# Kernel tuning notes

Hardware: AMD Instinct MI355X
Metric: run time of the kernel (lower is better)

## Reference

```python
import jax, jax.numpy as jnp
import numpy as np

DIM = 1024
LN_EPS = 1e-5

def _layernorm(x, w, b):
    m = jnp.mean(x, axis=-1, keepdims=True)
    v = jnp.mean((x - m) ** 2, axis=-1, keepdims=True)
    return (x - m) * jax.lax.rsqrt(v + LN_EPS) * w + b

def _linear(x, w, b):
    # torch Linear: w is (out, in)
    return jnp.einsum('bsd,od->bso', x, w) + b

def setup_inputs() -> dict:
    key = jax.random.key(0)
    ks = jax.random.split(key, 8)
    d = DIM
    s = 0.02
    return {
        'x': jax.random.normal(ks[0], (4, 4096, d), dtype=jnp.float32),
        'ln1_w': jnp.ones((d,), jnp.float32), 'ln1_b': jnp.zeros((d,), jnp.float32),
        'ln2_w': jnp.ones((d,), jnp.float32), 'ln2_b': jnp.zeros((d,), jnp.float32),
        'gate_w': jax.random.normal(ks[1], (d, d), jnp.float32) * s,
        'gate_b': jnp.zeros((d,), jnp.float32),
        'val_w': jax.random.normal(ks[2], (d, d), jnp.float32) * s,
        'val_b': jnp.zeros((d,), jnp.float32),
        'ffn1_w': jax.random.normal(ks[3], (4 * d, d), jnp.float32) * s,
        'ffn1_b': jnp.zeros((4 * d,), jnp.float32),
        'ffn2_w': jax.random.normal(ks[4], (d, 4 * d), jnp.float32) * s,
        'ffn2_b': jnp.zeros((d,), jnp.float32),
    }

def reference(x, ln1_w, ln1_b, ln2_w, ln2_b, gate_w, gate_b, val_w, val_b, ffn1_w, ffn1_b, ffn2_w, ffn2_b):
    batch, seq_len, dim = x.shape
    h = _layernorm(x, ln1_w, ln1_b)
    g = jax.nn.sigmoid(_linear(h, gate_w, gate_b))
    v = _linear(h, val_w, val_b)
    cumsum_v = jnp.cumsum(g * v, axis=1)
    cumsum_g = jnp.cumsum(g, axis=1) + 1e-6
    position = jnp.arange(1, seq_len + 1, dtype=x.dtype)[None, :, None]  # [1,S,1]
    mem = cumsum_v / (jnp.sqrt(cumsum_g) * jnp.sqrt(position / seq_len + 0.1))
    x = x + mem
    h2 = _layernorm(x, ln2_w, ln2_b)
    ff = _linear(jax.nn.gelu(_linear(h2, ffn1_w, ffn1_b), approximate=False), ffn2_w, ffn2_b)
    return x + ff
```

## Files before the change

kernel.cpp:

```cpp
#include <hip/hip_runtime.h>
#include <cstdint>
#include <cstddef>

#define DIMD 1024
#define SEQ  4096
#define BATCH 4
#define MTOT (BATCH*SEQ)
#define NCHUNK 64
#define CLEN   64

typedef __attribute__((ext_vector_type(8))) short short8;
typedef __attribute__((ext_vector_type(4))) float floatx4;

__device__ __forceinline__ unsigned short f2bf(float f){
  unsigned u = __float_as_uint(f);
  u += 0x7fffu + ((u >> 16) & 1u);
  return (unsigned short)(u >> 16);
}
__device__ __forceinline__ float bf2f(unsigned short u){
  return __uint_as_float((unsigned)u << 16);
}

__device__ __forceinline__ void async16(const void* g, void* l){
  __builtin_amdgcn_global_load_lds(
      (const __attribute__((address_space(1))) void*)g,
      (__attribute__((address_space(3))) void*)l, 16, 0, 0);
}

__global__ void f32_to_bf16_kernel(const float* __restrict__ in,
                                   unsigned short* __restrict__ out, int n){
  int i = (blockIdx.x * 256 + threadIdx.x) * 4;
  if (i < n){
    float4 v = *(const float4*)(in + i);
    uint2 o;
    o.x = (unsigned)f2bf(v.x) | ((unsigned)f2bf(v.y) << 16);
    o.y = (unsigned)f2bf(v.z) | ((unsigned)f2bf(v.w) << 16);
    *(uint2*)(out + i) = o;
  }
}

__global__ __launch_bounds__(256)
void ln_kernel(const float* __restrict__ X, const float* __restrict__ w,
               const float* __restrict__ b, unsigned short* __restrict__ H){
  const int row = blockIdx.x;
  const int tid = threadIdx.x;
  const float4 xv = ((const float4*)(X + (size_t)row * DIMD))[tid];
  float s  = xv.x + xv.y + xv.z + xv.w;
  float ss = xv.x*xv.x + xv.y*xv.y + xv.z*xv.z + xv.w*xv.w;
  #pragma unroll
  for (int o = 32; o; o >>= 1){
    s  += __shfl_down(s, o);
    ss += __shfl_down(ss, o);
  }
  __shared__ float ps[4], pss[4], mv[2];
  const int wid = tid >> 6, lane = tid & 63;
  if (lane == 0){ ps[wid] = s; pss[wid] = ss; }
  __syncthreads();
  if (tid == 0){
    float S1 = ps[0]+ps[1]+ps[2]+ps[3];
    float S2 = pss[0]+pss[1]+pss[2]+pss[3];
    float m = S1 * (1.0f / DIMD);
    float var = S2 * (1.0f / DIMD) - m*m;
    mv[0] = m; mv[1] = rsqrtf(var + 1e-5f);
  }
  __syncthreads();
  const float m = mv[0], rs = mv[1];
  const float4 wv = ((const float4*)w)[tid];
  const float4 bv = ((const float4*)b)[tid];
  float o0 = (xv.x - m) * rs * wv.x + bv.x;
  float o1 = (xv.y - m) * rs * wv.y + bv.y;
  float o2 = (xv.z - m) * rs * wv.z + bv.z;
  float o3 = (xv.w - m) * rs * wv.w + bv.w;
  uint2 o;
  o.x = (unsigned)f2bf(o0) | ((unsigned)f2bf(o1) << 16);
  o.y = (unsigned)f2bf(o2) | ((unsigned)f2bf(o3) << 16);
  ((uint2*)(H + (size_t)row * DIMD))[tid] = o;
}

template<int EPI>
__global__ __launch_bounds__(256, 4)
void gemm_bf16(const unsigned short* __restrict__ A, int lda,
               const unsigned short* __restrict__ Bw, int ldb,
               const float* __restrict__ bias, const float* __restrict__ bias2,
               void* __restrict__ OutP, void* __restrict__ Out2P,
               int ldc, int grid_n, int K)
{
  __shared__ unsigned short Alds[2][128*32];
  __shared__ unsigned short Blds[2][128*32];
  const int tid = threadIdx.x;
  const int bid = ((int)blockIdx.x & 7) * ((int)gridDim.x >> 3) + ((int)blockIdx.x >> 3);
  const int bm = bid / grid_n, bn = bid % grid_n;
  const int row0 = bm * 128, col0 = bn * 128;
  const int wid = tid >> 6, lane = tid & 63;
  const int wr = wid >> 1, wc = wid & 1;
  const int l15 = lane & 15, kh = (lane >> 4) * 8, rq = lane >> 4;

  const int idx0 = tid * 8;
  const int idx1 = 2048 + tid * 8;
  const int ar0 = idx0 >> 5, ac0 = idx0 & 31;
  const int ar1 = idx1 >> 5, ac1 = idx1 & 31;

  floatx4 acc[4][4];
  #pragma unroll
  for (int m = 0; m < 4; ++m)
    #pragma unroll
    for (int n = 0; n < 4; ++n)
      acc[m][n] = (floatx4){0.f, 0.f, 0.f, 0.f};

  auto stage = [&](int b, int k0){
    async16(A  + (size_t)(row0 + ar0) * lda + k0 + ac0, (char*)(&Alds[b][0]) + idx0*2);
    async16(A  + (size_t)(row0 + ar1) * lda + k0 + ac1, (char*)(&Alds[b][0]) + idx1*2);
    async16(Bw + (size_t)(col0 + ar0) * ldb + k0 + ac0, (char*)(&Blds[b][0]) + idx0*2);
    async16(Bw + (size_t)(col0 + ar1) * ldb + k0 + ac1, (char*)(&Blds[b][0]) + idx1*2);
  };
  auto compute = [&](int b){
    short8 af[4], bfr[4];
    #pragma unroll
    for (int m = 0; m < 4; ++m)
      af[m] = *(const short8*)(&Alds[b][(wr*64 + m*16 + l15)*32 + kh]);
    #pragma unroll
    for (int n = 0; n < 4; ++n)
      bfr[n] = *(const short8*)(&Blds[b][(wc*64 + n*16 + l15)*32 + kh]);
    #pragma unroll
    for (int m = 0; m < 4; ++m)
      #pragma unroll
      for (int n = 0; n < 4; ++n)
        acc[m][n] = __builtin_amdgcn_mfma_f32_16x16x32_bf16(af[m], bfr[n], acc[m][n], 0, 0, 0);
  };

  const int nt = K >> 5;
  stage(0, 0);
  __syncthreads();
  int cur = 0;
  for (int t = 0; t < nt - 1; ++t){
    stage(cur ^ 1, (t + 1) << 5);
    compute(cur);
    __syncthreads();
    cur ^= 1;
  }
  compute(cur);

  #pragma unroll
  for (int n = 0; n < 4; ++n){
    const int col = col0 + wc*64 + n*16 + l15;
    float bs;
    if constexpr (EPI == 4)      bs = 0.f;
    else if constexpr (EPI == 5) bs = (col < 1024) ? bias[col] : bias2[col - 1024];
    else                         bs = bias[col];
    #pragma unroll
    for (int m = 0; m < 4; ++m){
      const int rowb = row0 + wr*64 + m*16 + rq*4;
      #pragma unroll
      for (int j = 0; j < 4; ++j){
        const size_t o = (size_t)(rowb + j) * ldc + col;
        float val = acc[m][n][j] + bs;
        if constexpr (EPI == 2){
          ((unsigned short*)OutP)[o] = f2bf(0.5f * val * (1.f + erff(val * 0.70710678118f)));
        } else if constexpr (EPI == 3){
          float* O = (float*)OutP;
          O[o] = val + O[o];
        } else if constexpr (EPI == 4){
          float* O = (float*)OutP;
          O[o] = val + O[o];
        } else {
          if (col < 1024){
            ((unsigned short*)OutP)[(size_t)(rowb + j) * 1024 + col] =
                f2bf(1.f / (1.f + expf(-val)));
          } else {
            ((unsigned short*)Out2P)[(size_t)(rowb + j) * 1024 + (col - 1024)] =
                f2bf(val);
          }
        }
      }
    }
  }
}

__global__ __launch_bounds__(256)
void scan_sums(const unsigned short* __restrict__ G, const unsigned short* __restrict__ V,
               float* __restrict__ SG, float* __restrict__ SGV){
  const int bc = blockIdx.x;
  const int d  = blockIdx.y * 256 + threadIdx.x;
  const int b = bc >> 6, c = bc & 63;
  size_t base = ((size_t)b * SEQ + (size_t)c * CLEN) * DIMD + d;
  float sg = 0.f, sgv = 0.f;
  for (int i = 0; i < CLEN; ++i){
    float g = bf2f(G[base + (size_t)i * DIMD]);
    float v = bf2f(V[base + (size_t)i * DIMD]);
    sg += g; sgv += g * v;
  }
  SG[(size_t)bc * DIMD + d] = sg;
  SGV[(size_t)bc * DIMD + d] = sgv;
}

__global__ __launch_bounds__(256)
void scan_prefix(float* __restrict__ SG, float* __restrict__ SGV){
  const int b = blockIdx.x;
  const int d = blockIdx.y * 256 + threadIdx.x;
  float rg = 0.f, rgv = 0.f;
  for (int c = 0; c < NCHUNK; ++c){
    size_t i = ((size_t)(b * NCHUNK + c)) * DIMD + d;
    float tg = SG[i], tv = SGV[i];
    SG[i] = rg; SGV[i] = rgv;
    rg += tg; rgv += tv;
  }
}

__global__ __launch_bounds__(256)
void scan_final(const unsigned short* __restrict__ G, const unsigned short* __restrict__ V,
                const float* __restrict__ SG, const float* __restrict__ SGV,
                const float* __restrict__ X, float* __restrict__ X2){
  const int bc = blockIdx.x;
  const int d  = blockIdx.y * 256 + threadIdx.x;
  const int b = bc >> 6, c = bc & 63;
  size_t base = ((size_t)b * SEQ + (size_t)c * CLEN) * DIMD + d;
  float rg  = SG[(size_t)bc * DIMD + d];
  float rgv = SGV[(size_t)bc * DIMD + d];
  for (int i = 0; i < CLEN; ++i){
    size_t idx = base + (size_t)i * DIMD;
    float g = bf2f(G[idx]), v = bf2f(V[idx]);
    rg += g; rgv += g * v;
    int s = c * CLEN + i;
    float pf = (float)(s + 1) * (1.0f / SEQ) + 0.1f;
    float mem = rgv * rsqrtf((rg + 1e-6f) * pf);
    X2[idx] = X[idx] + mem;
  }
}

extern "C" void kernel_launch(void* const* d_in, const int* in_sizes, int n_in,
                              void* d_out, int out_size, void* d_ws, size_t ws_size,
                              hipStream_t stream)
{
  const float* x     = (const float*)d_in[0];
  const float* ln1w  = (const float*)d_in[1];
  const float* ln1b  = (const float*)d_in[2];
  const float* ln2w  = (const float*)d_in[3];
  const float* ln2b  = (const float*)d_in[4];
  const float* gatew = (const float*)d_in[5];
  const float* gateb = (const float*)d_in[6];
  const float* valw  = (const float*)d_in[7];
  const float* valb  = (const float*)d_in[8];
  const float* f1w   = (const float*)d_in[9];
  const float* f1b   = (const float*)d_in[10];
  const float* f2w   = (const float*)d_in[11];
  const float* f2b   = (const float*)d_in[12];
  float* out = (float*)d_out;

  const size_t MB = 1024u * 1024u;
  const size_t baseNeed = (size_t)(32+32+32+2+2+8+8)*MB + 2u*BATCH*NCHUNK*DIMD*4 + 4096;
  const bool bigT = (baseNeed + 64u*MB) <= ws_size;

  char* ws = (char*)d_ws;
  size_t off = 0;
  auto alloc = [&](size_t bytes) -> char* {
    char* p = ws + off; off += (bytes + 255) & ~(size_t)255; return p;
  };
  unsigned short* H  = (unsigned short*)alloc((size_t)MTOT * DIMD * 2);
  unsigned short* G  = (unsigned short*)alloc((size_t)MTOT * DIMD * 2);
  unsigned short* V  = (unsigned short*)alloc((size_t)MTOT * DIMD * 2);
  if (bigT) alloc(64u * MB);
  unsigned short* T  = G;
  unsigned short* WGV= (unsigned short*)alloc((size_t)2 * DIMD * DIMD * 2);
  unsigned short* W1 = (unsigned short*)alloc((size_t)4 * DIMD * DIMD * 2);
  unsigned short* W2 = (unsigned short*)alloc((size_t)4 * DIMD * DIMD * 2);
  float* SG  = (float*)alloc((size_t)BATCH * NCHUNK * DIMD * 4);
  float* SGV = (float*)alloc((size_t)BATCH * NCHUNK * DIMD * 4);

  if (off > ws_size) return;

  f32_to_bf16_kernel<<<DIMD*DIMD/1024, 256, 0, stream>>>(gatew, WGV, DIMD*DIMD);
  f32_to_bf16_kernel<<<DIMD*DIMD/1024, 256, 0, stream>>>(valw,  WGV + (size_t)DIMD*DIMD, DIMD*DIMD);
  f32_to_bf16_kernel<<<4*DIMD*DIMD/1024, 256, 0, stream>>>(f1w, W1, 4*DIMD*DIMD);
  f32_to_bf16_kernel<<<4*DIMD*DIMD/1024, 256, 0, stream>>>(f2w, W2, 4*DIMD*DIMD);

  ln_kernel<<<MTOT, 256, 0, stream>>>(x, ln1w, ln1b, H);

  gemm_bf16<5><<<(MTOT/128)*(2048/128), 256, 0, stream>>>(
      H, DIMD, WGV, DIMD, gateb, valb, G, V, 2048, 2048/128, DIMD);

  scan_sums  <<<dim3(BATCH*NCHUNK, DIMD/256), 256, 0, stream>>>(G, V, SG, SGV);
  scan_prefix<<<dim3(BATCH, DIMD/256),        256, 0, stream>>>(SG, SGV);
  scan_final <<<dim3(BATCH*NCHUNK, DIMD/256), 256, 0, stream>>>(G, V, SG, SGV, x, out);

  ln_kernel<<<MTOT, 256, 0, stream>>>(out, ln2w, ln2b, H);

  if (bigT){
    for (int c = 0; c < 2; ++c)
      gemm_bf16<2><<<(MTOT/128)*(2048/128), 256, 0, stream>>>(
          H, DIMD, W1 + (size_t)c*2048*DIMD, DIMD, f1b + c*2048, nullptr,
          T + (size_t)c*2048, nullptr, 4*DIMD, 2048/128, DIMD);
    gemm_bf16<3><<<(MTOT/128)*(DIMD/128), 256, 0, stream>>>(
        T, 4*DIMD, W2, 4*DIMD, f2b, nullptr, out, nullptr, DIMD, DIMD/128, 4*DIMD);
  } else {
    for (int c = 0; c < 2; ++c){
      const unsigned short* W1c = W1 + (size_t)c * 2048 * DIMD;
      const unsigned short* W2c = W2 + (size_t)c * 2048;
      gemm_bf16<2><<<(MTOT/128)*(2048/128), 256, 0, stream>>>(
          H, DIMD, W1c, DIMD, f1b + c*2048, nullptr, T, nullptr, 2048, 2048/128, DIMD);
      if (c == 0)
        gemm_bf16<3><<<(MTOT/128)*(DIMD/128), 256, 0, stream>>>(
            T, 2048, W2c, 4*DIMD, f2b, nullptr, out, nullptr, DIMD, DIMD/128, 2048);
      else
        gemm_bf16<4><<<(MTOT/128)*(DIMD/128), 256, 0, stream>>>(
            T, 2048, W2c, 4*DIMD, nullptr, nullptr, out, nullptr, DIMD, DIMD/128, 2048);
    }
  }
}
```

Baseline: 585.6 us.

## Replace 128x128 GEMM with 256x256 tile, 8-wave kernel using swizzled LDS

The bf16 MFMA GEMM moves from 128x128x32 tiles with 4 waves to 256x256x64 tiles with 8 waves. LDS loads now use an XOR swizzle to avoid bank conflicts, and the next K-tile is staged during the first quarter of compute, with s_setprio raised around the MFMA bursts. Larger tiles cut global and LDS traffic per FLOP. In exchange each wave holds 32 accumulators, which raises register pressure and lowers occupancy, and the grid has fewer blocks. With bigT, the FFN1 GEMM also runs as one launch instead of two.

```diff
diff --git a/kernel.cpp b/kernel.cpp
--- a/kernel.cpp
+++ b/kernel.cpp
@@ -78,78 +78,102 @@
 }
 
 template<int EPI>
-__global__ __launch_bounds__(256, 4)
-void gemm_bf16(const unsigned short* __restrict__ A, int lda,
-               const unsigned short* __restrict__ Bw, int ldb,
-               const float* __restrict__ bias, const float* __restrict__ bias2,
-               void* __restrict__ OutP, void* __restrict__ Out2P,
-               int ldc, int grid_n, int K)
+__global__ __launch_bounds__(512, 2)
+void gemm256(const unsigned short* __restrict__ A, int lda,
+             const unsigned short* __restrict__ Bw, int ldb,
+             const float* __restrict__ bias, const float* __restrict__ bias2,
+             void* __restrict__ OutP, void* __restrict__ Out2P,
+             int ldc, int grid_n, int K)
 {
-  __shared__ unsigned short Alds[2][128*32];
-  __shared__ unsigned short Blds[2][128*32];
+  __shared__ char lds[2][2][32*1024];
   const int tid = threadIdx.x;
   const int bid = ((int)blockIdx.x & 7) * ((int)gridDim.x >> 3) + ((int)blockIdx.x >> 3);
   const int bm = bid / grid_n, bn = bid % grid_n;
-  const int row0 = bm * 128, col0 = bn * 128;
+  const int row0 = bm * 256, col0 = bn * 256;
   const int wid = tid >> 6, lane = tid & 63;
-  const int wr = wid >> 1, wc = wid & 1;
-  const int l15 = lane & 15, kh = (lane >> 4) * 8, rq = lane >> 4;
-
-  const int idx0 = tid * 8;
-  const int idx1 = 2048 + tid * 8;
-  const int ar0 = idx0 >> 5, ac0 = idx0 & 31;
-  const int ar1 = idx1 >> 5, ac1 = idx1 & 31;
-
-  floatx4 acc[4][4];
+  const int wr = wid >> 2, wc = wid & 3;
+  const int l15 = lane & 15, rq = lane >> 4, l7 = lane & 7;
+
+  const int sbase = ((rq ^ (l7 & 3)) << 4) | (((l7 >> 2) & 1) << 6);
+
+  const int st_r  = tid >> 3;
+  const int st_sl = (tid & 7) ^ (st_r & 7);
+  const int st_ldsoff = tid * 16;
+
+  const unsigned short* Asrc = A  + (size_t)(row0 + st_r) * lda + st_sl * 8;
+  const unsigned short* Bsrc = Bw + (size_t)(col0 + st_r) * ldb + st_sl * 8;
+
+  floatx4 acc[8][4];
   #pragma unroll
-  for (int m = 0; m < 4; ++m)
+  for (int m = 0; m < 8; ++m)
     #pragma unroll
     for (int n = 0; n < 4; ++n)
       acc[m][n] = (floatx4){0.f, 0.f, 0.f, 0.f};
 
-  auto stage = [&](int b, int k0){
-    async16(A  + (size_t)(row0 + ar0) * lda + k0 + ac0, (char*)(&Alds[b][0]) + idx0*2);
-    async16(A  + (size_t)(row0 + ar1) * lda + k0 + ac1, (char*)(&Alds[b][0]) + idx1*2);
-    async16(Bw + (size_t)(col0 + ar0) * ldb + k0 + ac0, (char*)(&Blds[b][0]) + idx0*2);
-    async16(Bw + (size_t)(col0 + ar1) * ldb + k0 + ac1, (char*)(&Blds[b][0]) + idx1*2);
+  auto stage = [&](int buf, int k0){
+    #pragma unroll
+    for (int i = 0; i < 4; ++i)
+      async16(Asrc + (size_t)(i * 64) * lda + k0, &lds[buf][0][i * 8192 + st_ldsoff]);
+    #pragma unroll
+    for (int i = 0; i < 4; ++i)
+      async16(Bsrc + (size_t)(i * 64) * ldb + k0, &lds[buf][1][i * 8192 + st_ldsoff]);
   };
-  auto compute = [&](int b){
-    short8 af[4], bfr[4];
-    #pragma unroll
-    for (int m = 0; m < 4; ++m)
-      af[m] = *(const short8*)(&Alds[b][(wr*64 + m*16 + l15)*32 + kh]);
-    #pragma unroll
-    for (int n = 0; n < 4; ++n)
-      bfr[n] = *(const short8*)(&Blds[b][(wc*64 + n*16 + l15)*32 + kh]);
-    #pragma unroll
-    for (int m = 0; m < 4; ++m)
+
+  const int nt = K >> 6;
+  stage(0, 0);
+  asm volatile("s_waitcnt vmcnt(0)" ::: "memory");
+  asm volatile("s_barrier" ::: "memory");
+
+  for (int t = 0; t < nt; ++t){
+    const int buf = t & 1;
+    const char* La = &lds[buf][0][0];
+    const char* Lb = &lds[buf][1][0];
+    #pragma unroll
+    for (int q = 0; q < 4; ++q){
+      const int qm = q >> 1, qn = q & 1;
+      short8 af[4][2], bfv[2][2];
       #pragma unroll
-      for (int n = 0; n < 4; ++n)
-        acc[m][n] = __builtin_amdgcn_mfma_f32_16x16x32_bf16(af[m], bfr[n], acc[m][n], 0, 0, 0);
-  };
-
-  const int nt = K >> 5;
-  stage(0, 0);
-  __syncthreads();
-  int cur = 0;
-  for (int t = 0; t < nt - 1; ++t){
-    stage(cur ^ 1, (t + 1) << 5);
-    compute(cur);
-    __syncthreads();
-    cur ^= 1;
-  }
-  compute(cur);
+      for (int mi = 0; mi < 4; ++mi){
+        const int r = wr * 128 + (qm * 4 + mi) * 16 + l15;
+        #pragma unroll
+        for (int ks = 0; ks < 2; ++ks)
+          af[mi][ks] = *(const short8*)(La + r * 128 + (sbase ^ (ks << 6)));
+      }
+      #pragma unroll
+      for (int ni = 0; ni < 2; ++ni){
+        const int r = wc * 64 + (qn * 2 + ni) * 16 + l15;
+        #pragma unroll
+        for (int ks = 0; ks < 2; ++ks)
+          bfv[ni][ks] = *(const short8*)(Lb + r * 128 + (sbase ^ (ks << 6)));
+      }
+      if (q == 0 && t + 1 < nt) stage(buf ^ 1, (t + 1) << 6);
+      asm volatile("s_barrier" ::: "memory");
+      __builtin_amdgcn_s_setprio(1);
+      #pragma unroll
+      for (int mi = 0; mi < 4; ++mi)
+        #pragma unroll
+        for (int ni = 0; ni < 2; ++ni)
+          #pragma unroll
+          for (int ks = 0; ks < 2; ++ks)
+            acc[qm*4+mi][qn*2+ni] = __builtin_amdgcn_mfma_f32_16x16x32_bf16(
+                af[mi][ks], bfv[ni][ks], acc[qm*4+mi][qn*2+ni], 0, 0, 0);
+      __builtin_amdgcn_s_setprio(0);
+      if (q == 3)
+        asm volatile("s_waitcnt vmcnt(0)" ::: "memory");
+      asm volatile("s_barrier" ::: "memory");
+    }
+  }
 
   #pragma unroll
   for (int n = 0; n < 4; ++n){
-    const int col = col0 + wc*64 + n*16 + l15;
+    const int col = col0 + wc * 64 + n * 16 + l15;
     float bs;
     if constexpr (EPI == 4)      bs = 0.f;
     else if constexpr (EPI == 5) bs = (col < 1024) ? bias[col] : bias2[col - 1024];
     else                         bs = bias[col];
     #pragma unroll
-    for (int m = 0; m < 4; ++m){
-      const int rowb = row0 + wr*64 + m*16 + rq*4;
+    for (int m = 0; m < 8; ++m){
+      const int rowb = row0 + wr * 128 + m * 16 + rq * 4;
       #pragma unroll
       for (int j = 0; j < 4; ++j){
         const size_t o = (size_t)(rowb + j) * ldc + col;
@@ -275,8 +299,8 @@
 
   ln_kernel<<<MTOT, 256, 0, stream>>>(x, ln1w, ln1b, H);
 
-  gemm_bf16<5><<<(MTOT/128)*(2048/128), 256, 0, stream>>>(
-      H, DIMD, WGV, DIMD, gateb, valb, G, V, 2048, 2048/128, DIMD);
+  gemm256<5><<<(MTOT/256)*(2048/256), 512, 0, stream>>>(
+      H, DIMD, WGV, DIMD, gateb, valb, G, V, 2048, 2048/256, DIMD);
 
   scan_sums  <<<dim3(BATCH*NCHUNK, DIMD/256), 256, 0, stream>>>(G, V, SG, SGV);
   scan_prefix<<<dim3(BATCH, DIMD/256),        256, 0, stream>>>(SG, SGV);
@@ -285,24 +309,22 @@
   ln_kernel<<<MTOT, 256, 0, stream>>>(out, ln2w, ln2b, H);
 
   if (bigT){
-    for (int c = 0; c < 2; ++c)
-      gemm_bf16<2><<<(MTOT/128)*(2048/128), 256, 0, stream>>>(
-          H, DIMD, W1 + (size_t)c*2048*DIMD, DIMD, f1b + c*2048, nullptr,
-          T + (size_t)c*2048, nullptr, 4*DIMD, 2048/128, DIMD);
-    gemm_bf16<3><<<(MTOT/128)*(DIMD/128), 256, 0, stream>>>(
-        T, 4*DIMD, W2, 4*DIMD, f2b, nullptr, out, nullptr, DIMD, DIMD/128, 4*DIMD);
+    gemm256<2><<<(MTOT/256)*(4096/256), 512, 0, stream>>>(
+        H, DIMD, W1, DIMD, f1b, nullptr, T, nullptr, 4*DIMD, 4096/256, DIMD);
+    gemm256<3><<<(MTOT/256)*(DIMD/256), 512, 0, stream>>>(
+        T, 4*DIMD, W2, 4*DIMD, f2b, nullptr, out, nullptr, DIMD, DIMD/256, 4*DIMD);
   } else {
     for (int c = 0; c < 2; ++c){
       const unsigned short* W1c = W1 + (size_t)c * 2048 * DIMD;
       const unsigned short* W2c = W2 + (size_t)c * 2048;
-      gemm_bf16<2><<<(MTOT/128)*(2048/128), 256, 0, stream>>>(
-          H, DIMD, W1c, DIMD, f1b + c*2048, nullptr, T, nullptr, 2048, 2048/128, DIMD);
+      gemm256<2><<<(MTOT/256)*(2048/256), 512, 0, stream>>>(
+          H, DIMD, W1c, DIMD, f1b + c*2048, nullptr, T, nullptr, 2048, 2048/256, DIMD);
       if (c == 0)
-        gemm_bf16<3><<<(MTOT/128)*(DIMD/128), 256, 0, stream>>>(
-            T, 2048, W2c, 4*DIMD, f2b, nullptr, out, nullptr, DIMD, DIMD/128, 2048);
+        gemm256<3><<<(MTOT/256)*(DIMD/256), 512, 0, stream>>>(
+            T, 2048, W2c, 4*DIMD, f2b, nullptr, out, nullptr, DIMD, DIMD/256, 2048);
       else
-        gemm_bf16<4><<<(MTOT/128)*(DIMD/128), 256, 0, stream>>>(
-            T, 2048, W2c, 4*DIMD, nullptr, nullptr, out, nullptr, DIMD, DIMD/128, 2048);
+        gemm256<4><<<(MTOT/256)*(DIMD/256), 512, 0, stream>>>(
+            T, 2048, W2c, 4*DIMD, nullptr, nullptr, out, nullptr, DIMD, DIMD/256, 2048);
     }
   }
 }
```

Result: slower. 635.0 us (+8.4%).

## Stage bf16 GEMM epilogue through swizzled LDS for coalesced 16-byte stores

Applied to the files above, without the earlier changes.

For the gate/value and FFN1 GEMMs, the epilogue now writes the activated bf16 results into a per-wave XOR-swizzled LDS slab and reads them back as 16-byte rows. Global stores then go out as wide coalesced writes instead of scattered 2-byte stores. The extra 16KB of shared memory per block lowers the occupancy hint from 4 to 3 blocks. The two FFN1 launches on the large-buffer path are merged into a single launch over all 4096 columns.

```diff
diff --git a/kernel.cpp b/kernel.cpp
--- a/kernel.cpp
+++ b/kernel.cpp
@@ -78,7 +78,7 @@
 }
 
 template<int EPI>
-__global__ __launch_bounds__(256, 4)
+__global__ __launch_bounds__(256, 3)
 void gemm_bf16(const unsigned short* __restrict__ A, int lda,
                const unsigned short* __restrict__ Bw, int ldb,
                const float* __restrict__ bias, const float* __restrict__ bias2,
@@ -87,6 +87,7 @@
 {
   __shared__ unsigned short Alds[2][128*32];
   __shared__ unsigned short Blds[2][128*32];
+  __shared__ char slab[4][4096];
   const int tid = threadIdx.x;
   const int bid = ((int)blockIdx.x & 7) * ((int)gridDim.x >> 3) + ((int)blockIdx.x >> 3);
   const int bm = bid / grid_n, bn = bid % grid_n;
@@ -140,36 +141,63 @@
   }
   compute(cur);
 
-  #pragma unroll
-  for (int n = 0; n < 4; ++n){
-    const int col = col0 + wc*64 + n*16 + l15;
-    float bs;
-    if constexpr (EPI == 4)      bs = 0.f;
-    else if constexpr (EPI == 5) bs = (col < 1024) ? bias[col] : bias2[col - 1024];
-    else                         bs = bias[col];
+  if constexpr (EPI == 2 || EPI == 5){
+    __syncthreads();
+    char* sl = &slab[wid][0];
+    unsigned short* dst; int colw; int ldout; bool sigm = false;
+    const float* bsel;
+    if constexpr (EPI == 5){
+      const int c0 = col0 + wc * 64;
+      if (c0 < 1024){ dst = (unsigned short*)OutP;  colw = c0;        bsel = bias;  sigm = true;  }
+      else          { dst = (unsigned short*)Out2P; colw = c0 - 1024; bsel = bias2; sigm = false; }
+      ldout = 1024;
+    } else {
+      dst = (unsigned short*)OutP; colw = col0 + wc * 64; bsel = bias; ldout = ldc;
+    }
+    const int rdrow = lane >> 3;
+    const int rdoff  = rdrow * 128 + (((lane & 7) ^ (rdrow & 7)) << 4);
+    const int rdoff2 = (rdrow + 8) * 128 + (((lane & 7) ^ ((rdrow + 8) & 7)) << 4);
+    const int rdsl = (lane & 7) * 16;
     #pragma unroll
     for (int m = 0; m < 4; ++m){
-      const int rowb = row0 + wr*64 + m*16 + rq*4;
       #pragma unroll
-      for (int j = 0; j < 4; ++j){
-        const size_t o = (size_t)(rowb + j) * ldc + col;
-        float val = acc[m][n][j] + bs;
-        if constexpr (EPI == 2){
-          ((unsigned short*)OutP)[o] = f2bf(0.5f * val * (1.f + erff(val * 0.70710678118f)));
-        } else if constexpr (EPI == 3){
+      for (int n = 0; n < 4; ++n){
+        const float bs = bsel[colw + n*16 + l15];
+        const int cchunk = n*2 + (l15 >> 3);
+        #pragma unroll
+        for (int j = 0; j < 4; ++j){
+          const float val = acc[m][n][j] + bs;
+          float r;
+          if constexpr (EPI == 2){
+            r = 0.5f * val * (1.f + erff(val * 0.70710678118f));
+          } else {
+            r = sigm ? (1.f / (1.f + expf(-val))) : val;
+          }
+          const int rr = rq*4 + j;
+          *(unsigned short*)(sl + rr*128 + ((cchunk ^ (rr & 7)) << 4) + (l15 & 7)*2) = f2bf(r);
+        }
+      }
+      asm volatile("s_waitcnt lgkmcnt(0)" ::: "memory");
+      uint4 w0 = *(const uint4*)(sl + rdoff);
+      uint4 w1 = *(const uint4*)(sl + rdoff2);
+      asm volatile("s_waitcnt lgkmcnt(0)" ::: "memory");
+      const int growb = row0 + wr * 64 + m * 16;
+      *(uint4*)((char*)(dst + (size_t)(growb + rdrow) * ldout + colw) + rdsl) = w0;
+      *(uint4*)((char*)(dst + (size_t)(growb + rdrow + 8) * ldout + colw) + rdsl) = w1;
+    }
+  } else {
+    #pragma unroll
+    for (int n = 0; n < 4; ++n){
+      const int col = col0 + wc * 64 + n * 16 + l15;
+      const float bs = (EPI == 4) ? 0.f : bias[col];
+      #pragma unroll
+      for (int m = 0; m < 4; ++m){
+        const int rowb = row0 + wr * 64 + m * 16 + rq * 4;
+        #pragma unroll
+        for (int j = 0; j < 4; ++j){
+          const size_t o = (size_t)(rowb + j) * ldc + col;
           float* O = (float*)OutP;
-          O[o] = val + O[o];
-        } else if constexpr (EPI == 4){
-          float* O = (float*)OutP;
-          O[o] = val + O[o];
-        } else {
-          if (col < 1024){
-            ((unsigned short*)OutP)[(size_t)(rowb + j) * 1024 + col] =
-                f2bf(1.f / (1.f + expf(-val)));
-          } else {
-            ((unsigned short*)Out2P)[(size_t)(rowb + j) * 1024 + (col - 1024)] =
-                f2bf(val);
-          }
+          O[o] = acc[m][n][j] + bs + O[o];
         }
       }
     }
@@ -285,10 +313,8 @@
   ln_kernel<<<MTOT, 256, 0, stream>>>(out, ln2w, ln2b, H);
 
   if (bigT){
-    for (int c = 0; c < 2; ++c)
-      gemm_bf16<2><<<(MTOT/128)*(2048/128), 256, 0, stream>>>(
-          H, DIMD, W1 + (size_t)c*2048*DIMD, DIMD, f1b + c*2048, nullptr,
-          T + (size_t)c*2048, nullptr, 4*DIMD, 2048/128, DIMD);
+    gemm_bf16<2><<<(MTOT/128)*(4096/128), 256, 0, stream>>>(
+        H, DIMD, W1, DIMD, f1b, nullptr, T, nullptr, 4*DIMD, 4096/128, DIMD);
     gemm_bf16<3><<<(MTOT/128)*(DIMD/128), 256, 0, stream>>>(
         T, 4*DIMD, W2, 4*DIMD, f2b, nullptr, out, nullptr, DIMD, DIMD/128, 4*DIMD);
   } else {
```

Measured after the change: 599.0 us. 2.3% more time.
